# Kernel optimization log

Hardware: AMD Instinct MI355X
Metric: run time of the kernel (lower is better)

The kernel has to match this reference:

```python
import jax, jax.numpy as jnp
import numpy as np

HIDDEN = 2048
N_HEADS = 16
N_KV = 2
HEAD_DIM = 256
PARTIAL = 0.25
ROT = int(HEAD_DIM * PARTIAL)  # 64
BATCH, SEQ = 1, 4096
NEG = -1e9


def apply_partial_rope(x, cos, sin):
    # x: (b, s, h, d); rotate first ROT dims (rotate-half convention), pass rest through.
    x_rot, x_pass = x[..., :ROT], x[..., ROT:]
    half = ROT // 2
    x1, x2 = x_rot[..., :half], x_rot[..., half:]
    c = cos[None, :, None, :]  # (1, s, 1, rot/2)
    s = sin[None, :, None, :]
    rotated = jnp.concatenate([x1 * c - x2 * s, x1 * s + x2 * c], axis=-1)
    return jnp.concatenate([rotated, x_pass], axis=-1)


def setup_inputs() -> dict:
    key = jax.random.key(0)
    ks = jax.random.split(key, 6)
    hidden_states = jax.random.normal(ks[0], (BATCH, SEQ, HIDDEN), dtype=jnp.float32)
    # RoPE tables: theta = 10000^{-2i/rot}
    inv_freq = 1.0 / (10000.0 ** (np.arange(0, ROT, 2, dtype=np.float32) / ROT))
    ang = np.arange(SEQ, dtype=np.float32)[:, None] * inv_freq[None, :]  # (s, rot/2)
    cos = jnp.asarray(np.cos(ang))
    sin = jnp.asarray(np.sin(ang))
    # causal mask (1,1,s,s)
    mask = jnp.triu(jnp.full((SEQ, SEQ), NEG, dtype=jnp.float32), k=1)[None, None]
    scale = 0.02
    wq = jax.random.normal(ks[1], (HIDDEN, N_HEADS * HEAD_DIM), dtype=jnp.float32) * scale
    wk = jax.random.normal(ks[2], (HIDDEN, N_KV * HEAD_DIM), dtype=jnp.float32) * scale
    wv = jax.random.normal(ks[3], (HIDDEN, N_KV * HEAD_DIM), dtype=jnp.float32) * scale
    wo = jax.random.normal(ks[4], (N_HEADS * HEAD_DIM, HIDDEN), dtype=jnp.float32) * scale
    return {"hidden_states": hidden_states, "cos": cos, "sin": sin,
            "attention_mask": mask, "wq": wq, "wk": wk, "wv": wv, "wo": wo}


def reference(hidden_states, cos, sin, attention_mask, wq, wk, wv, wo):
    b, s, _ = hidden_states.shape
    g = N_HEADS // N_KV
    scale = HEAD_DIM ** -0.5
    q = (hidden_states @ wq).reshape(b, s, N_HEADS, HEAD_DIM)
    k = (hidden_states @ wk).reshape(b, s, N_KV, HEAD_DIM)
    v = (hidden_states @ wv).reshape(b, s, N_KV, HEAD_DIM)
    q = apply_partial_rope(q, cos, sin)
    k = apply_partial_rope(k, cos, sin)
    new_k, new_v = k, v  # kv cache (no prior cache)
    # GQA without repeat_interleave: group q heads by their kv head.
    # repeat_interleave maps q head h -> kv head h // g, matching this reshape.
    qg = q.reshape(b, s, N_KV, g, HEAD_DIM)
    scores = jnp.einsum('bqkgd,blkd->bkgql', qg, k) * scale  # (b, kv, g, s, s)
    scores = scores + attention_mask[:, :, None]  # broadcast (b,1,1,s,s)
    probs = jax.nn.softmax(scores.astype(jnp.float32), axis=-1).astype(q.dtype)
    ctx = jnp.einsum('bkgql,blkd->bqkgd', probs, v)  # (b, s, kv, g, d)
    attn_out = ctx.reshape(b, s, N_HEADS * HEAD_DIM)
    output = attn_out @ wo
    return output, new_k, new_v
```

## Files before the change

kernel.cpp:

```cpp
#include <hip/hip_runtime.h>
#include <hip/hip_bf16.h>

typedef __bf16 bf16;
typedef bf16 bf16x8 __attribute__((ext_vector_type(8)));
typedef bf16 bf16x4 __attribute__((ext_vector_type(4)));
typedef float f32x4 __attribute__((ext_vector_type(4)));

#define SEQ    4096
#define HIDDEN 2048
#define NHEADS 16
#define NKV    2
#define HDIM   256
#define ROTD   64
#define ROTH   32
#define QN     (NHEADS*HDIM)
#define KVN    (NKV*HDIM)

typedef __attribute__((address_space(3))) unsigned int lds_u32;
typedef const __attribute__((address_space(1))) unsigned int glb_u32;
__device__ __forceinline__ void async_copy16(const void* g, void* l) {
  __builtin_amdgcn_global_load_lds((glb_u32*)g, (lds_u32*)l, 16, 0, 0);
}

__global__ __launch_bounds__(256) void convert_f32_bf16(
    const float* __restrict__ in, bf16* __restrict__ out, int n)
{
  int i = (blockIdx.x * 256 + threadIdx.x) * 4;
  if (i >= n) return;
  f32x4 v = *(const f32x4*)(in + i);
  bf16x4 o;
  #pragma unroll
  for (int j = 0; j < 4; j++) o[j] = (bf16)v[j];
  *(bf16x4*)(out + i) = o;
}

template<typename T>
__global__ __launch_bounds__(256) void transpose_to_bf16(
    const T* __restrict__ in, bf16* __restrict__ out, int R, int C)
{
  __shared__ float tile[32][33];
  int bx = blockIdx.x * 32;
  int by = blockIdx.y * 32;
  int tx = threadIdx.x & 31, ty = threadIdx.x >> 5;
  #pragma unroll
  for (int i = 0; i < 4; i++)
    tile[ty + i*8][tx] = (float)in[(size_t)(by + ty + i*8) * C + bx + tx];
  __syncthreads();
  #pragma unroll
  for (int i = 0; i < 4; i++)
    out[(size_t)(bx + ty + i*8) * R + by + tx] = (bf16)tile[tx][ty + i*8];
}

template<bool WF32, bool WBF16>
__global__ __launch_bounds__(256) void gemm_bt(
    const bf16* __restrict__ A, const bf16* __restrict__ Bt,
    float* __restrict__ Cf, bf16* __restrict__ Cb,
    int M, int N, int K)
{
  const int bm = blockIdx.y * 128;
  const int bn = blockIdx.x * 128;
  const int tid = threadIdx.x;
  const int wave = tid >> 6, lane = tid & 63;
  const int l16 = lane & 15, quad = lane >> 4;
  const int wr = (wave & 1) * 64;
  const int wc = (wave >> 1) * 64;

  __shared__ bf16 As[128*32];
  __shared__ bf16 Bs[128*32];

  f32x4 acc[4][4];
  #pragma unroll
  for (int r = 0; r < 4; r++)
    #pragma unroll
    for (int c = 0; c < 4; c++) acc[r][c] = (f32x4){0.f,0.f,0.f,0.f};

  const int arow = tid >> 2;
  const int acol = (tid & 3) * 8;
  const bf16* ag0 = A  + (size_t)(bm + arow)      * K + acol;
  const bf16* ag1 = A  + (size_t)(bm + 64 + arow) * K + acol;
  const bf16* bg0 = Bt + (size_t)(bn + arow)      * K + acol;
  const bf16* bg1 = Bt + (size_t)(bn + 64 + arow) * K + acol;
  bf16* la = As + tid*8;
  bf16* lb = Bs + tid*8;

  for (int kk = 0; kk < K; kk += 32) {
    __syncthreads();
    async_copy16(ag0 + kk, la);
    async_copy16(ag1 + kk, la + 2048);
    async_copy16(bg0 + kk, lb);
    async_copy16(bg1 + kk, lb + 2048);
    __syncthreads();

    bf16x8 af[4], bfr[4];
    #pragma unroll
    for (int r = 0; r < 4; r++) af[r]  = *(const bf16x8*)&As[(wr + r*16 + l16)*32 + quad*8];
    #pragma unroll
    for (int c = 0; c < 4; c++) bfr[c] = *(const bf16x8*)&Bs[(wc + c*16 + l16)*32 + quad*8];
    #pragma unroll
    for (int r = 0; r < 4; r++)
      #pragma unroll
      for (int c = 0; c < 4; c++)
        acc[r][c] = __builtin_amdgcn_mfma_f32_16x16x32_bf16(af[r], bfr[c], acc[r][c], 0, 0, 0);
  }

  #pragma unroll
  for (int r = 0; r < 4; r++)
    #pragma unroll
    for (int c = 0; c < 4; c++)
      #pragma unroll
      for (int rr = 0; rr < 4; rr++) {
        size_t idx = (size_t)(bm + wr + r*16 + quad*4 + rr) * N + bn + wc + c*16 + l16;
        if (WF32)  Cf[idx] = acc[r][c][rr];
        if (WBF16) Cb[idx] = (bf16)acc[r][c][rr];
      }
}

#define G256_STG(gp, stride, lbase, b, h, kt) do {                            \
    async_copy16((gp) + (size_t)((h)*128     ) * (stride) + (size_t)(kt)*64,  \
                 (lbase) + (b)*16384 + (h)*8192);                             \
    async_copy16((gp) + (size_t)((h)*128 + 64) * (stride) + (size_t)(kt)*64,  \
                 (lbase) + (b)*16384 + (h)*8192 + 4096);                      \
  } while (0)

#define G256_DSA(b, P) do {                                                   \
    _Pragma("unroll")                                                         \
    for (int m2 = 0; m2 < 2; m2++) {                                          \
      const int ro = (b)*16384 + arow0 + ((P)*2 + m2) * 1024;                 \
      af[m2][0] = *(const bf16x8*)&smem[ro + fc0];                            \
      af[m2][1] = *(const bf16x8*)&smem[ro + fc1];                            \
    }                                                                         \
  } while (0)

#define G256_DSB(b) do {                                                      \
    _Pragma("unroll")                                                         \
    for (int n4 = 0; n4 < 4; n4++) {                                          \
      const int ro = 32768 + (b)*16384 + brow0 + n4 * 1024;                   \
      bq[n4][0] = *(const bf16x8*)&smem[ro + fc0];                            \
      bq[n4][1] = *(const bf16x8*)&smem[ro + fc1];                            \
    }                                                                         \
  } while (0)

#define G256_MM(P) do {                                                       \
    _Pragma("unroll")                                                         \
    for (int m2 = 0; m2 < 2; m2++)                                            \
      _Pragma("unroll")                                                       \
      for (int n4 = 0; n4 < 4; n4++) {                                        \
        acc[(P)*2+m2][n4] = __builtin_amdgcn_mfma_f32_16x16x32_bf16(          \
            af[m2][0], bq[n4][0], acc[(P)*2+m2][n4], 0, 0, 0);                \
        acc[(P)*2+m2][n4] = __builtin_amdgcn_mfma_f32_16x16x32_bf16(          \
            af[m2][1], bq[n4][1], acc[(P)*2+m2][n4], 0, 0, 0);                \
      }                                                                       \
  } while (0)

#define G256_BAR  __builtin_amdgcn_s_barrier()
#define G256_WLG  do { asm volatile("s_waitcnt lgkmcnt(0)" ::: "memory");     \
                       __builtin_amdgcn_sched_barrier(0); } while (0)

template<bool WF32, bool WBF16>
__global__ __launch_bounds__(512, 2) void gemm256(
    const bf16* __restrict__ A, const bf16* __restrict__ Bt,
    float* __restrict__ Cf0, float* __restrict__ Cf1, bf16* __restrict__ Cb,
    int N, int K, int lda, int ldb)
{
  const int gx = gridDim.x;
  const int nwg = gx * gridDim.y;
  int wg = blockIdx.y * gx + blockIdx.x;
  wg = (wg & 7) * (nwg >> 3) + (wg >> 3);
  const int bn = (wg % gx) * 256;
  const int bm = (wg / gx) * 256;

  const int z = blockIdx.z;
  A  += (size_t)z * K;
  Bt += (size_t)z * K;
  float* __restrict__ Cf = z ? Cf1 : Cf0;

  const int tid = threadIdx.x;
  const int lane = tid & 63;
  const int l16 = lane & 15, quad = lane >> 4;
  const int wv = tid >> 6;
  const int wm = wv >> 2;
  const int wn = wv & 3;

  __shared__ bf16 smem[65536];

  const int srow = tid >> 3;
  const int scol = ((tid & 7) ^ (srow & 7)) << 3;
  const bf16* Ag = A  + (size_t)(bm + srow) * lda + scol;
  const bf16* Bg = Bt + (size_t)(bn + srow) * ldb + scol;
  bf16* lA = smem + tid * 8;
  bf16* lB = smem + 32768 + tid * 8;

  const int fsw = l16 & 7;
  const int fc0 = ((quad       ^ fsw) << 3);
  const int fc1 = (((4 + quad) ^ fsw) << 3);
  const int arow0 = (wm * 128 + l16) * 64;
  const int brow0 = (wn * 64  + l16) * 64;

  f32x4 acc[8][4];
  #pragma unroll
  for (int m = 0; m < 8; m++)
    #pragma unroll
    for (int n = 0; n < 4; n++) acc[m][n] = (f32x4){0.f,0.f,0.f,0.f};

  const int niter = K >> 7;

  G256_STG(Ag, lda, lA, 0, 0, 0);  G256_STG(Ag, lda, lA, 0, 1, 0);
  G256_STG(Bg, ldb, lB, 0, 0, 0);  G256_STG(Bg, ldb, lB, 0, 1, 0);
  G256_STG(Bg, ldb, lB, 1, 0, 1);  G256_STG(Bg, ldb, lB, 1, 1, 1);
  asm volatile("s_waitcnt vmcnt(4)" ::: "memory");
  G256_BAR;

  bf16x8 af[2][2];
  bf16x8 bq[4][2];

  for (int i = 0; i < niter; i++) {
    const int O = 2*i + 1;
    const bool nl = (i + 1 < niter);

    G256_DSB(0); G256_DSA(0, 0);
    G256_STG(Ag, lda, lA, 1, 0, O);
    G256_BAR; G256_WLG;
    __builtin_amdgcn_s_setprio(1); G256_MM(0); __builtin_amdgcn_s_setprio(0);
    G256_BAR;
    G256_DSA(0, 1);
    G256_STG(Ag, lda, lA, 1, 1, O);
    G256_BAR; G256_WLG;
    __builtin_amdgcn_s_setprio(1); G256_MM(1); __builtin_amdgcn_s_setprio(0);
    G256_BAR;
    G256_DSA(0, 2);
    if (nl) G256_STG(Bg, ldb, lB, 0, 0, O+1);
    G256_BAR; G256_WLG;
    __builtin_amdgcn_s_setprio(1); G256_MM(2); __builtin_amdgcn_s_setprio(0);
    G256_BAR;
    G256_DSA(0, 3);
    if (nl) G256_STG(Bg, ldb, lB, 0, 1, O+1);
    G256_BAR; G256_WLG;
    __builtin_amdgcn_s_setprio(1); G256_MM(3); __builtin_amdgcn_s_setprio(0);
    if (nl) asm volatile("s_waitcnt vmcnt(4)" ::: "memory");
    else    asm volatile("s_waitcnt vmcnt(0)" ::: "memory");
    G256_BAR;
    G256_DSB(1); G256_DSA(1, 0);
    if (nl) G256_STG(Ag, lda, lA, 0, 0, O+1);
    G256_BAR; G256_WLG;
    __builtin_amdgcn_s_setprio(1); G256_MM(0); __builtin_amdgcn_s_setprio(0);
    G256_BAR;
    G256_DSA(1, 1);
    if (nl) G256_STG(Ag, lda, lA, 0, 1, O+1);
    G256_BAR; G256_WLG;
    __builtin_amdgcn_s_setprio(1); G256_MM(1); __builtin_amdgcn_s_setprio(0);
    G256_BAR;
    G256_DSA(1, 2);
    if (nl) G256_STG(Bg, ldb, lB, 1, 0, O+2);
    G256_BAR; G256_WLG;
    __builtin_amdgcn_s_setprio(1); G256_MM(2); __builtin_amdgcn_s_setprio(0);
    G256_BAR;
    G256_DSA(1, 3);
    if (nl) G256_STG(Bg, ldb, lB, 1, 1, O+2);
    G256_BAR; G256_WLG;
    __builtin_amdgcn_s_setprio(1); G256_MM(3); __builtin_amdgcn_s_setprio(0);
    if (nl) asm volatile("s_waitcnt vmcnt(4)" ::: "memory");
    G256_BAR;
  }

  #pragma unroll
  for (int mf = 0; mf < 8; mf++)
    #pragma unroll
    for (int n = 0; n < 4; n++)
      #pragma unroll
      for (int rr = 0; rr < 4; rr++) {
        size_t idx = (size_t)(bm + wm*128 + mf*16 + quad*4 + rr) * N
                   + bn + wn*64 + n*16 + l16;
        if (WF32)  Cf[idx] = acc[mf][n][rr];
        if (WBF16) Cb[idx] = (bf16)acc[mf][n][rr];
      }
}

__global__ __launch_bounds__(256) void add_f32(
    const float* __restrict__ a, float* __restrict__ b, int n)
{
  int i = (blockIdx.x * 256 + threadIdx.x) * 4;
  if (i >= n) return;
  f32x4 x = *(const f32x4*)(a + i);
  f32x4 y = *(const f32x4*)(b + i);
  #pragma unroll
  for (int j = 0; j < 4; j++) y[j] += x[j];
  *(f32x4*)(b + i) = y;
}

__global__ __launch_bounds__(256) void rope_kernel(
    bf16* __restrict__ Q, bf16* __restrict__ K,
    const float* __restrict__ cosb, const float* __restrict__ sinb,
    float* __restrict__ newk)
{
  int s = blockIdx.x;
  int t = threadIdx.x;
  __shared__ float cf[ROTH], sf[ROTH];
  if (t < ROTH) { cf[t] = cosb[s*ROTH + t]; sf[t] = sinb[s*ROTH + t]; }
  __syncthreads();

  float qv[4];
  #pragma unroll
  for (int i = 0; i < 4; i++) {
    int w = t + 256*i;
    int h = w >> 6, d = w & 63;
    size_t base = ((size_t)s*NHEADS + h)*HDIM;
    if (d < ROTH) {
      float x1 = (float)Q[base + d], x2 = (float)Q[base + d + ROTH];
      qv[i] = x1*cf[d] - x2*sf[d];
    } else {
      int dd = d - ROTH;
      float x1 = (float)Q[base + dd], x2 = (float)Q[base + d];
      qv[i] = x1*sf[dd] + x2*cf[dd];
    }
  }
  float kvv[2];
  #pragma unroll
  for (int i = 0; i < 2; i++) {
    int w = t + 256*i;
    int h = w >> 8, d = w & 255;
    size_t base = ((size_t)s*NKV + h)*HDIM;
    if (d < ROTH) {
      kvv[i] = (float)K[base + d]*cf[d] - (float)K[base + d + ROTH]*sf[d];
    } else if (d < ROTD) {
      int dd = d - ROTH;
      kvv[i] = (float)K[base + dd]*sf[dd] + (float)K[base + d]*cf[dd];
    } else {
      kvv[i] = (float)K[base + d];
    }
  }
  __syncthreads();
  #pragma unroll
  for (int i = 0; i < 4; i++) {
    int w = t + 256*i;
    int h = w >> 6, d = w & 63;
    Q[((size_t)s*NHEADS + h)*HDIM + d] = (bf16)qv[i];
  }
  #pragma unroll
  for (int i = 0; i < 2; i++) {
    int w = t + 256*i;
    int h = w >> 8, d = w & 255;
    size_t base = ((size_t)s*NKV + h)*HDIM;
    K[base + d]    = (bf16)kvv[i];
    newk[base + d] = kvv[i];
  }
}

__global__ __launch_bounds__(512, 2) void attn_v7(
    const bf16* __restrict__ Q, const bf16* __restrict__ Kc,
    const bf16* __restrict__ Vt, bf16* __restrict__ ctx)
{
  const int qs  = blockIdx.x;
  const int hp  = blockIdx.y;
  const int kvh = hp >> 2;
  const int tid = threadIdx.x, wave = tid >> 6, lane = tid & 63;
  const int l16 = lane & 15, quad = lane >> 4;
  const int h   = hp*2 + (wave >> 2);
  const int q0  = qs*128 + (wave & 3)*32;

  __shared__ bf16 Ks[2][64*256];
  __shared__ bf16 Vs[2][256*64];
  __shared__ bf16 PsAll[8][32][40];
  bf16 (*Ps)[40] = PsAll[wave];

  bf16x8 aq[2][8];
  #pragma unroll
  for (int u = 0; u < 2; u++) {
    const bf16* qp = Q + (size_t)(q0 + u*16 + l16)*QN + h*HDIM + quad*8;
    #pragma unroll
    for (int c = 0; c < 8; c++) aq[u][c] = *(const bf16x8*)(qp + c*32);
  }

  f32x4 o[2][16];
  #pragma unroll
  for (int u = 0; u < 2; u++)
    #pragma unroll
    for (int c = 0; c < 16; c++) o[u][c] = (f32x4){0.f,0.f,0.f,0.f};
  float lsum[2][4] = {{0.f,0.f,0.f,0.f},{0.f,0.f,0.f,0.f}};

  const int krow0 = tid >> 5;
  const int kcg   = ((tid & 31) ^ (krow0 & 7)) * 8;
  const bf16* kg  = Kc + (size_t)kvh*HDIM + kcg;
  const int vd0 = tid >> 3;
  const int vcg = ((tid & 7) ^ (vd0 & 7)) * 8;
  const bf16* vg  = Vt + (size_t)(kvh*HDIM + vd0)*SEQ + vcg;

  const int ntiles = qs*2 + 2;

  #define ATTN_STAGE(t, b) do {                                               \
    const int _l0 = (t)*64;                                                   \
    bf16* _ks = &Ks[b][0] + tid*8;                                            \
    bf16* _vs = &Vs[b][0] + tid*8;                                            \
    _Pragma("unroll")                                                         \
    for (int p = 0; p < 4; p++) {                                             \
      async_copy16(kg + (size_t)(_l0 + p*16 + krow0)*KVN, _ks + p*4096);      \
      async_copy16(vg + (size_t)(p*64)*SEQ + _l0,         _vs + p*4096);      \
    }                                                                         \
  } while (0)

  ATTN_STAGE(0, 0);
  ATTN_STAGE(1, 1);
  asm volatile("s_waitcnt vmcnt(8)" ::: "memory");
  __builtin_amdgcn_s_barrier();

  const float C1 = 0.09016844f;
  const float C0 = -17.31234050f;

  for (int t = 0; t < ntiles; t++) {
    const int b  = t & 1;
    const int l0 = t*64;

    #pragma unroll
    for (int hh = 0; hh < 2; hh++) {
      const int l0h = l0 + hh*32;
      if (l0h <= q0 + 31) {
        f32x4 s2[2][2];
        #pragma unroll
        for (int u = 0; u < 2; u++)
          #pragma unroll
          for (int t4 = 0; t4 < 2; t4++) s2[u][t4] = (f32x4){0.f,0.f,0.f,0.f};
        __builtin_amdgcn_s_setprio(1);
        #pragma unroll
        for (int c = 0; c < 8; c++) {
          const int cs = ((c*4 + quad) ^ (l16 & 7)) * 8;
          #pragma unroll
          for (int t4 = 0; t4 < 2; t4++) {
            bf16x8 kb = *(const bf16x8*)&Ks[b][(hh*32 + t4*16 + l16)*256 + cs];
            #pragma unroll
            for (int u = 0; u < 2; u++)
              s2[u][t4] = __builtin_amdgcn_mfma_f32_16x16x32_bf16(aq[u][c], kb, s2[u][t4], 0, 0, 0);
          }
        }
        __builtin_amdgcn_s_setprio(0);

        const bool need_mask = (l0h + 31 > q0);
        #pragma unroll
        for (int u = 0; u < 2; u++)
          #pragma unroll
          for (int rr = 0; rr < 4; rr++) {
            const int row = q0 + u*16 + quad*4 + rr;
            float p0 = exp2f(fmaf(s2[u][0][rr], C1, C0));
            float p1 = exp2f(fmaf(s2[u][1][rr], C1, C0));
            if (need_mask) {
              if (l0h +      l16 > row) p0 = 0.f;
              if (l0h + 16 + l16 > row) p1 = 0.f;
            }
            lsum[u][rr] += p0 + p1;
            Ps[u*16 + quad*4 + rr][l16]      = (bf16)p0;
            Ps[u*16 + quad*4 + rr][16 + l16] = (bf16)p1;
          }

        bf16x8 pa[2];
        #pragma unroll
        for (int u = 0; u < 2; u++) pa[u] = *(const bf16x8*)&Ps[u*16 + l16][quad*8];
        const int vs = (((hh*4 + quad) ^ (l16 & 7))) * 8;
        __builtin_amdgcn_s_setprio(1);
        #pragma unroll
        for (int c = 0; c < 16; c++) {
          bf16x8 vb = *(const bf16x8*)&Vs[b][(c*16 + l16)*64 + vs];
          #pragma unroll
          for (int u = 0; u < 2; u++)
            o[u][c] = __builtin_amdgcn_mfma_f32_16x16x32_bf16(pa[u], vb, o[u][c], 0, 0, 0);
        }
        __builtin_amdgcn_s_setprio(0);
      }
    }

    if (t + 1 < ntiles) {
      __builtin_amdgcn_s_barrier();
      if (t + 2 < ntiles) {
        ATTN_STAGE(t + 2, b);
        asm volatile("s_waitcnt vmcnt(8)" ::: "memory");
      } else {
        asm volatile("s_waitcnt vmcnt(0)" ::: "memory");
      }
      __builtin_amdgcn_s_barrier();
    }
  }
  #undef ATTN_STAGE

  #pragma unroll
  for (int u = 0; u < 2; u++)
    #pragma unroll
    for (int rr = 0; rr < 4; rr++) {
      float l = lsum[u][rr];
      l += __shfl_xor(l, 1);
      l += __shfl_xor(l, 2);
      l += __shfl_xor(l, 4);
      l += __shfl_xor(l, 8);
      float inv = 1.0f / l;
      size_t base = (size_t)(q0 + u*16 + quad*4 + rr)*QN + h*HDIM;
      #pragma unroll
      for (int c = 0; c < 16; c++)
        ctx[base + c*16 + l16] = (bf16)(o[u][c][rr] * inv);
    }
}

extern "C" void kernel_launch(void* const* d_in, const int* in_sizes, int n_in,
                              void* d_out, int out_size, void* d_ws, size_t ws_size,
                              hipStream_t stream)
{
  const float* X    = (const float*)d_in[0];
  const float* cosb = (const float*)d_in[1];
  const float* sinb = (const float*)d_in[2];
  const float* wq   = (const float*)d_in[4];
  const float* wk   = (const float*)d_in[5];
  const float* wv   = (const float*)d_in[6];
  const float* wo   = (const float*)d_in[7];

  float* out  = (float*)d_out;
  float* newk = out  + (size_t)SEQ*HIDDEN;
  float* newv = newk + (size_t)SEQ*KVN;

  bf16* Xb  = (bf16*)d_ws;
  bf16* wqT = Xb  + (size_t)SEQ*HIDDEN;
  bf16* Qb  = wqT + (size_t)QN*HIDDEN;
  bf16* Kb  = Qb  + (size_t)SEQ*QN;
  bf16* Vb  = Kb  + (size_t)SEQ*KVN;
  bf16* Vt  = Vb  + (size_t)SEQ*KVN;
  bf16* wkT = Vt  + (size_t)KVN*SEQ;
  bf16* wvT = wkT + (size_t)KVN*HIDDEN;
  bf16* woT = wvT + (size_t)KVN*HIDDEN;
  bf16* ctx = Xb;
  float* part = (float*)Qb;

  dim3 blk(256);
  convert_f32_bf16<<<dim3(SEQ*HIDDEN/1024), blk, 0, stream>>>(X, Xb, SEQ*HIDDEN);
  transpose_to_bf16<float><<<dim3(QN/32,     HIDDEN/32), blk, 0, stream>>>(wq, wqT, HIDDEN, QN);
  transpose_to_bf16<float><<<dim3(KVN/32,    HIDDEN/32), blk, 0, stream>>>(wk, wkT, HIDDEN, KVN);
  transpose_to_bf16<float><<<dim3(KVN/32,    HIDDEN/32), blk, 0, stream>>>(wv, wvT, HIDDEN, KVN);
  transpose_to_bf16<float><<<dim3(HIDDEN/32, QN/32),     blk, 0, stream>>>(wo, woT, QN, HIDDEN);

  gemm256<false,true><<<dim3(QN/256, SEQ/256, 1), dim3(512), 0, stream>>>(
      Xb, wqT, nullptr, nullptr, Qb, QN, HIDDEN, HIDDEN, HIDDEN);
  gemm_bt<false,true><<<dim3(KVN/128, SEQ/128), blk, 0, stream>>>(Xb, wkT, nullptr, Kb, SEQ, KVN, HIDDEN);
  gemm_bt<true, true><<<dim3(KVN/128, SEQ/128), blk, 0, stream>>>(Xb, wvT, newv,   Vb, SEQ, KVN, HIDDEN);

  rope_kernel<<<dim3(SEQ), blk, 0, stream>>>(Qb, Kb, cosb, sinb, newk);
  transpose_to_bf16<bf16><<<dim3(KVN/32, SEQ/32), blk, 0, stream>>>(Vb, Vt, SEQ, KVN);

  attn_v7<<<dim3(SEQ/128, NHEADS/2), dim3(512), 0, stream>>>(Qb, Kb, Vt, ctx);

  gemm256<true,false><<<dim3(HIDDEN/256, SEQ/256, 2), dim3(512), 0, stream>>>(
      ctx, woT, out, part, nullptr, HIDDEN, QN/2, QN, QN);
  add_f32<<<dim3(SEQ*HIDDEN/1024), blk, 0, stream>>>(part, out, SEQ*HIDDEN);
}
```

Before: 738.7 us.

## Balance causal attention by splitting key ranges and pairing query blocks

Each attention block now handles two work items. One is the low half of the key range for query block ib; the other is the high half of the key range for query block 31-ib. This gives every block about the same number of key tiles, instead of the triangular spread that made the last blocks run far longer than the first. Each half writes unnormalized partial outputs (fp32 when workspace allows, otherwise bf16) and its row sums. A new merge kernel adds the two halves and normalizes. The cost is extra global memory traffic for the partials and an added kernel launch.

```diff
diff --git a/kernel.cpp b/kernel.cpp
--- a/kernel.cpp
+++ b/kernel.cpp
@@ -345,37 +345,23 @@
   }
 }
 
-__global__ __launch_bounds__(512, 2) void attn_v7(
+__global__ __launch_bounds__(512, 2) void attn_v8(
     const bf16* __restrict__ Q, const bf16* __restrict__ Kc,
-    const bf16* __restrict__ Vt, bf16* __restrict__ ctx)
-{
-  const int qs  = blockIdx.x;
+    const bf16* __restrict__ Vt,
+    void* __restrict__ oLo, void* __restrict__ oHi,
+    float* __restrict__ lLo, float* __restrict__ lHi, int use_f32)
+{
+  const int ib  = blockIdx.x;
   const int hp  = blockIdx.y;
   const int kvh = hp >> 2;
   const int tid = threadIdx.x, wave = tid >> 6, lane = tid & 63;
   const int l16 = lane & 15, quad = lane >> 4;
   const int h   = hp*2 + (wave >> 2);
-  const int q0  = qs*128 + (wave & 3)*32;
 
   __shared__ bf16 Ks[2][64*256];
   __shared__ bf16 Vs[2][256*64];
   __shared__ bf16 PsAll[8][32][40];
   bf16 (*Ps)[40] = PsAll[wave];
-
-  bf16x8 aq[2][8];
-  #pragma unroll
-  for (int u = 0; u < 2; u++) {
-    const bf16* qp = Q + (size_t)(q0 + u*16 + l16)*QN + h*HDIM + quad*8;
-    #pragma unroll
-    for (int c = 0; c < 8; c++) aq[u][c] = *(const bf16x8*)(qp + c*32);
-  }
-
-  f32x4 o[2][16];
-  #pragma unroll
-  for (int u = 0; u < 2; u++)
-    #pragma unroll
-    for (int c = 0; c < 16; c++) o[u][c] = (f32x4){0.f,0.f,0.f,0.f};
-  float lsum[2][4] = {{0.f,0.f,0.f,0.f},{0.f,0.f,0.f,0.f}};
 
   const int krow0 = tid >> 5;
   const int kcg   = ((tid & 31) ^ (krow0 & 7)) * 8;
@@ -383,8 +369,6 @@
   const int vd0 = tid >> 3;
   const int vcg = ((tid & 7) ^ (vd0 & 7)) * 8;
   const bf16* vg  = Vt + (size_t)(kvh*HDIM + vd0)*SEQ + vcg;
-
-  const int ntiles = qs*2 + 2;
 
   #define ATTN_STAGE(t, b) do {                                               \
     const int _l0 = (t)*64;                                                   \
@@ -397,102 +381,166 @@
     }                                                                         \
   } while (0)
 
-  ATTN_STAGE(0, 0);
-  ATTN_STAGE(1, 1);
-  asm volatile("s_waitcnt vmcnt(8)" ::: "memory");
-  __builtin_amdgcn_s_barrier();
-
   const float C1 = 0.09016844f;
   const float C0 = -17.31234050f;
 
-  for (int t = 0; t < ntiles; t++) {
-    const int b  = t & 1;
-    const int l0 = t*64;
-
-    #pragma unroll
-    for (int hh = 0; hh < 2; hh++) {
-      const int l0h = l0 + hh*32;
-      if (l0h <= q0 + 31) {
-        f32x4 s2[2][2];
-        #pragma unroll
-        for (int u = 0; u < 2; u++)
+  for (int cc = 0; cc < 2; cc++) {
+    const int qs = cc ? (31 - ib) : ib;
+    const int t0 = cc ? (32 - ib)  : 0;
+    const int t1 = cc ? (64 - 2*ib) : (ib + 1);
+    const int q0 = qs*128 + (wave & 3)*32;
+
+    bf16x8 aq[2][8];
+    #pragma unroll
+    for (int u = 0; u < 2; u++) {
+      const bf16* qp = Q + (size_t)(q0 + u*16 + l16)*QN + h*HDIM + quad*8;
+      #pragma unroll
+      for (int c = 0; c < 8; c++) aq[u][c] = *(const bf16x8*)(qp + c*32);
+    }
+
+    f32x4 o[2][16];
+    #pragma unroll
+    for (int u = 0; u < 2; u++)
+      #pragma unroll
+      for (int c = 0; c < 16; c++) o[u][c] = (f32x4){0.f,0.f,0.f,0.f};
+    float lsum[2][4] = {{0.f,0.f,0.f,0.f},{0.f,0.f,0.f,0.f}};
+
+    ATTN_STAGE(t0, 0);
+    ATTN_STAGE(t0 + 1, 1);
+    asm volatile("s_waitcnt vmcnt(8)" ::: "memory");
+    __builtin_amdgcn_s_barrier();
+
+    for (int t = t0; t < t1; t++) {
+      const int b  = (t - t0) & 1;
+      const int l0 = t*64;
+
+      #pragma unroll
+      for (int hh = 0; hh < 2; hh++) {
+        const int l0h = l0 + hh*32;
+        if (l0h <= q0 + 31) {
+          f32x4 s2[2][2];
           #pragma unroll
-          for (int t4 = 0; t4 < 2; t4++) s2[u][t4] = (f32x4){0.f,0.f,0.f,0.f};
-        __builtin_amdgcn_s_setprio(1);
-        #pragma unroll
-        for (int c = 0; c < 8; c++) {
-          const int cs = ((c*4 + quad) ^ (l16 & 7)) * 8;
+          for (int u = 0; u < 2; u++)
+            #pragma unroll
+            for (int t4 = 0; t4 < 2; t4++) s2[u][t4] = (f32x4){0.f,0.f,0.f,0.f};
+          __builtin_amdgcn_s_setprio(1);
           #pragma unroll
-          for (int t4 = 0; t4 < 2; t4++) {
-            bf16x8 kb = *(const bf16x8*)&Ks[b][(hh*32 + t4*16 + l16)*256 + cs];
+          for (int c = 0; c < 8; c++) {
+            const int cs = ((c*4 + quad) ^ (l16 & 7)) * 8;
+            #pragma unroll
+            for (int t4 = 0; t4 < 2; t4++) {
+              bf16x8 kb = *(const bf16x8*)&Ks[b][(hh*32 + t4*16 + l16)*256 + cs];
+              #pragma unroll
+              for (int u = 0; u < 2; u++)
+                s2[u][t4] = __builtin_amdgcn_mfma_f32_16x16x32_bf16(aq[u][c], kb, s2[u][t4], 0, 0, 0);
+            }
+          }
+          __builtin_amdgcn_s_setprio(0);
+
+          const bool need_mask = (l0h + 31 > q0);
+          #pragma unroll
+          for (int u = 0; u < 2; u++)
+            #pragma unroll
+            for (int rr = 0; rr < 4; rr++) {
+              const int row = q0 + u*16 + quad*4 + rr;
+              float p0 = exp2f(fmaf(s2[u][0][rr], C1, C0));
+              float p1 = exp2f(fmaf(s2[u][1][rr], C1, C0));
+              if (need_mask) {
+                if (l0h +      l16 > row) p0 = 0.f;
+                if (l0h + 16 + l16 > row) p1 = 0.f;
+              }
+              lsum[u][rr] += p0 + p1;
+              Ps[u*16 + quad*4 + rr][l16]      = (bf16)p0;
+              Ps[u*16 + quad*4 + rr][16 + l16] = (bf16)p1;
+            }
+
+          bf16x8 pa[2];
+          #pragma unroll
+          for (int u = 0; u < 2; u++) pa[u] = *(const bf16x8*)&Ps[u*16 + l16][quad*8];
+          const int vs = (((hh*4 + quad) ^ (l16 & 7))) * 8;
+          __builtin_amdgcn_s_setprio(1);
+          #pragma unroll
+          for (int c = 0; c < 16; c++) {
+            bf16x8 vb = *(const bf16x8*)&Vs[b][(c*16 + l16)*64 + vs];
             #pragma unroll
             for (int u = 0; u < 2; u++)
-              s2[u][t4] = __builtin_amdgcn_mfma_f32_16x16x32_bf16(aq[u][c], kb, s2[u][t4], 0, 0, 0);
+              o[u][c] = __builtin_amdgcn_mfma_f32_16x16x32_bf16(pa[u], vb, o[u][c], 0, 0, 0);
           }
+          __builtin_amdgcn_s_setprio(0);
         }
-        __builtin_amdgcn_s_setprio(0);
-
-        const bool need_mask = (l0h + 31 > q0);
-        #pragma unroll
-        for (int u = 0; u < 2; u++)
-          #pragma unroll
-          for (int rr = 0; rr < 4; rr++) {
-            const int row = q0 + u*16 + quad*4 + rr;
-            float p0 = exp2f(fmaf(s2[u][0][rr], C1, C0));
-            float p1 = exp2f(fmaf(s2[u][1][rr], C1, C0));
-            if (need_mask) {
-              if (l0h +      l16 > row) p0 = 0.f;
-              if (l0h + 16 + l16 > row) p1 = 0.f;
-            }
-            lsum[u][rr] += p0 + p1;
-            Ps[u*16 + quad*4 + rr][l16]      = (bf16)p0;
-            Ps[u*16 + quad*4 + rr][16 + l16] = (bf16)p1;
-          }
-
-        bf16x8 pa[2];
-        #pragma unroll
-        for (int u = 0; u < 2; u++) pa[u] = *(const bf16x8*)&Ps[u*16 + l16][quad*8];
-        const int vs = (((hh*4 + quad) ^ (l16 & 7))) * 8;
-        __builtin_amdgcn_s_setprio(1);
-        #pragma unroll
-        for (int c = 0; c < 16; c++) {
-          bf16x8 vb = *(const bf16x8*)&Vs[b][(c*16 + l16)*64 + vs];
-          #pragma unroll
-          for (int u = 0; u < 2; u++)
-            o[u][c] = __builtin_amdgcn_mfma_f32_16x16x32_bf16(pa[u], vb, o[u][c], 0, 0, 0);
+      }
+
+      if (t + 1 < t1) {
+        __builtin_amdgcn_s_barrier();
+        if (t + 2 < t1) {
+          ATTN_STAGE(t + 2, b);
+          asm volatile("s_waitcnt vmcnt(8)" ::: "memory");
+        } else {
+          asm volatile("s_waitcnt vmcnt(0)" ::: "memory");
         }
-        __builtin_amdgcn_s_setprio(0);
+        __builtin_amdgcn_s_barrier();
       }
     }
 
-    if (t + 1 < ntiles) {
-      __builtin_amdgcn_s_barrier();
-      if (t + 2 < ntiles) {
-        ATTN_STAGE(t + 2, b);
-        asm volatile("s_waitcnt vmcnt(8)" ::: "memory");
-      } else {
-        asm volatile("s_waitcnt vmcnt(0)" ::: "memory");
+    void*  osl = cc ? oHi : oLo;
+    float* lsl = cc ? lHi : lLo;
+    #pragma unroll
+    for (int u = 0; u < 2; u++)
+      #pragma unroll
+      for (int rr = 0; rr < 4; rr++) {
+        float l = lsum[u][rr];
+        l += __shfl_xor(l, 1);
+        l += __shfl_xor(l, 2);
+        l += __shfl_xor(l, 4);
+        l += __shfl_xor(l, 8);
+        const int row = q0 + u*16 + quad*4 + rr;
+        size_t base = (size_t)row*QN + h*HDIM;
+        if (use_f32) {
+          float* po = (float*)osl;
+          #pragma unroll
+          for (int c = 0; c < 16; c++) po[base + c*16 + l16] = o[u][c][rr];
+        } else {
+          bf16* po = (bf16*)osl;
+          #pragma unroll
+          for (int c = 0; c < 16; c++) po[base + c*16 + l16] = (bf16)o[u][c][rr];
+        }
+        if (l16 == 0) lsl[row*NHEADS + h] = l;
       }
-      __builtin_amdgcn_s_barrier();
-    }
+
+    asm volatile("s_waitcnt vmcnt(0)" ::: "memory");
+    __builtin_amdgcn_s_barrier();
   }
   #undef ATTN_STAGE
-
-  #pragma unroll
-  for (int u = 0; u < 2; u++)
-    #pragma unroll
-    for (int rr = 0; rr < 4; rr++) {
-      float l = lsum[u][rr];
-      l += __shfl_xor(l, 1);
-      l += __shfl_xor(l, 2);
-      l += __shfl_xor(l, 4);
-      l += __shfl_xor(l, 8);
-      float inv = 1.0f / l;
-      size_t base = (size_t)(q0 + u*16 + quad*4 + rr)*QN + h*HDIM;
-      #pragma unroll
-      for (int c = 0; c < 16; c++)
-        ctx[base + c*16 + l16] = (bf16)(o[u][c][rr] * inv);
-    }
+}
+
+template<bool F32>
+__global__ __launch_bounds__(256) void merge_attn(
+    const void* __restrict__ oLo, const void* __restrict__ oHi,
+    const float* __restrict__ lLo, const float* __restrict__ lHi,
+    bf16* __restrict__ ctx)
+{
+  size_t flat = ((size_t)blockIdx.x * 256 + threadIdx.x) * 8;
+  int row = (int)(flat >> 12);
+  int h   = (int)((flat >> 8) & 15);
+  float inv = 1.0f / (lLo[row*NHEADS + h] + lHi[row*NHEADS + h]);
+  float a[8], b[8];
+  if (F32) {
+    const float* pl = (const float*)oLo + flat;
+    const float* ph = (const float*)oHi + flat;
+    f32x4 a0 = *(const f32x4*)pl, a1 = *(const f32x4*)(pl + 4);
+    f32x4 b0 = *(const f32x4*)ph, b1 = *(const f32x4*)(ph + 4);
+    #pragma unroll
+    for (int j = 0; j < 4; j++) { a[j] = a0[j]; a[4+j] = a1[j]; b[j] = b0[j]; b[4+j] = b1[j]; }
+  } else {
+    bf16x8 a8 = *(const bf16x8*)((const bf16*)oLo + flat);
+    bf16x8 b8 = *(const bf16x8*)((const bf16*)oHi + flat);
+    #pragma unroll
+    for (int j = 0; j < 8; j++) { a[j] = (float)a8[j]; b[j] = (float)b8[j]; }
+  }
+  bf16x8 r;
+  #pragma unroll
+  for (int j = 0; j < 8; j++) r[j] = (bf16)((a[j] + b[j]) * inv);
+  *(bf16x8*)(ctx + flat) = r;
 }
 
 extern "C" void kernel_launch(void* const* d_in, const int* in_sizes, int n_in,
@@ -523,6 +571,20 @@
   bf16* ctx = Xb;
   float* part = (float*)Qb;
 
+  const size_t base_bytes = (size_t)96 * 1024 * 1024;
+  const size_t f32_slot   = (size_t)SEQ * QN * sizeof(float);
+  const int use_f32 = (ws_size >= base_bytes + 2*f32_slot) ? 1 : 0;
+  void* oLo; void* oHi;
+  if (use_f32) {
+    oLo = (char*)d_ws + base_bytes;
+    oHi = (char*)d_ws + base_bytes + f32_slot;
+  } else {
+    oLo = (void*)out;
+    oHi = (void*)ctx;
+  }
+  float* lLo = (float*)wkT;
+  float* lHi = lLo + (size_t)SEQ*NHEADS;
+
   dim3 blk(256);
   convert_f32_bf16<<<dim3(SEQ*HIDDEN/1024), blk, 0, stream>>>(X, Xb, SEQ*HIDDEN);
   transpose_to_bf16<float><<<dim3(QN/32,     HIDDEN/32), blk, 0, stream>>>(wq, wqT, HIDDEN, QN);
@@ -538,7 +600,12 @@
   rope_kernel<<<dim3(SEQ), blk, 0, stream>>>(Qb, Kb, cosb, sinb, newk);
   transpose_to_bf16<bf16><<<dim3(KVN/32, SEQ/32), blk, 0, stream>>>(Vb, Vt, SEQ, KVN);
 
-  attn_v7<<<dim3(SEQ/128, NHEADS/2), dim3(512), 0, stream>>>(Qb, Kb, Vt, ctx);
+  attn_v8<<<dim3(32, 8), dim3(512), 0, stream>>>(Qb, Kb, Vt, oLo, oHi, lLo, lHi, use_f32);
+
+  if (use_f32)
+    merge_attn<true ><<<dim3(SEQ*QN/8/256), blk, 0, stream>>>(oLo, oHi, lLo, lHi, ctx);
+  else
+    merge_attn<false><<<dim3(SEQ*QN/8/256), blk, 0, stream>>>(oLo, oHi, lLo, lHi, ctx);
 
   gemm256<true,false><<<dim3(HIDDEN/256, SEQ/256, 2), dim3(512), 0, stream>>>(
       ctx, woT, out, part, nullptr, HIDDEN, QN/2, QN, QN);
```

Result: faster. 645.0 us (-12.7%).
